# Kernel tuning notes

Measured on AMD Instinct MI355X. Metric: run time of the kernel, lower is better.

Reference implementation:

```python
import jax, jax.numpy as jnp
import numpy as np


def rotate_half(x):
    # interleaved rotate: (x0,x1,x2,x3,...) -> (-x1,x0,-x3,x2,...)
    x1 = x[..., 0::2]
    x2 = x[..., 1::2]
    return jnp.stack((-x2, x1), axis=-1).reshape(x.shape)


def setup_inputs() -> dict:
    key = jax.random.key(0)
    B, T, C, H = 8, 2048, 2048, 128
    ks = jax.random.split(key, 4)
    x = jax.random.normal(ks[0], (B, T, C), dtype=jnp.float32)
    wq = jax.random.normal(ks[1], (C, H), dtype=jnp.float32) * (C ** -0.5)
    wk = jax.random.normal(ks[2], (C, H), dtype=jnp.float32) * (C ** -0.5)
    wv = jax.random.normal(ks[3], (C, H), dtype=jnp.float32) * (C ** -0.5)
    # standard RoPE tables, interleaved pairs share a frequency
    inv_freq = 1.0 / (10000.0 ** (np.arange(0, H, 2, dtype=np.float32) / H))  # [H/2]
    ang = np.arange(T, dtype=np.float32)[:, None] * inv_freq[None, :]          # [T, H/2]
    ang = np.repeat(ang, 2, axis=-1)                                           # [T, H]
    rope_cos = jnp.asarray(np.cos(ang), dtype=jnp.float32)
    rope_sin = jnp.asarray(np.sin(ang), dtype=jnp.float32)
    return {"x": x, "wq": wq, "wk": wk, "wv": wv,
            "rope_cos": rope_cos, "rope_sin": rope_sin}


def reference(x, wq, wk, wv, rope_cos, rope_sin):
    B, T, C = x.shape
    H = wq.shape[1]
    q = x @ wq  # [B,T,H]
    k = x @ wk
    cos = rope_cos[:T][None]  # [1,T,H]
    sin = rope_sin[:T][None]
    q = q * cos + rotate_half(q) * sin
    k = k * cos + rotate_half(k) * sin
    wei = jnp.einsum('bth,bsh->bts', q, k) / (H ** 0.5)  # [B,T,T]
    causal = jnp.tril(jnp.ones((T, T), dtype=bool))
    wei = jnp.where(causal[None], wei, -jnp.inf)
    wei = jax.nn.softmax(wei, axis=-1)
    v = x @ wv  # [B,T,H]
    out = jnp.einsum('bts,bsh->bth', wei, v)
    return out
```

## Files before the change

### kernel.cpp

```cpp
#include <hip/hip_runtime.h>
#include <hip/hip_bf16.h>

typedef __attribute__((ext_vector_type(8))) short bf16x8;
typedef __attribute__((ext_vector_type(8))) unsigned short u16x8;
typedef __attribute__((ext_vector_type(4))) unsigned short u16x4;
typedef __attribute__((ext_vector_type(4))) float f32x4;

__device__ __forceinline__ unsigned short f2bf(float f) {
    __hip_bfloat16 h = __float2bfloat16(f);
    return *reinterpret_cast<unsigned short*>(&h);
}

__device__ __forceinline__ void cp16(void* lds, const void* g) {
    __builtin_amdgcn_global_load_lds(
        (const __attribute__((address_space(1))) unsigned int*)g,
        (__attribute__((address_space(3))) unsigned int*)lds, 16, 0, 0);
}

__global__ __launch_bounds__(256) void pack_w(
    const float* __restrict__ wq, const float* __restrict__ wk,
    const float* __restrict__ wv, unsigned short* __restrict__ wt)
{
    int idx = blockIdx.x * 256 + threadIdx.x;
    int n   = idx & 127;
    int k   = (idx >> 7) & 2047;
    int sel = idx >> 18;
    const float* w = (sel == 0) ? wq : (sel == 1) ? wk : wv;
    wt[(size_t)(sel * 128 + n) * 2048 + k] = f2bf(w[k * 128 + n]);
}

__global__ __launch_bounds__(256) void qkv_gemm(
    const float* __restrict__ x, const unsigned short* __restrict__ wt,
    const float* __restrict__ rc, const float* __restrict__ rs,
    unsigned short* __restrict__ Qb, unsigned short* __restrict__ Kb,
    unsigned short* __restrict__ VT)
{
    __shared__ __align__(16) unsigned short As[2][128 * 32];
    __shared__ __align__(16) unsigned short Bs[2][128 * 32];

    const int bid   = blockIdx.x;
    const int slot  = bid & 7;
    const int idx   = bid >> 3;
    const int mtile = slot + 8 * (idx / 3);
    const int ntile = idx % 3;

    const int tid  = threadIdx.x;
    const int lane = tid & 63;
    const int wid  = tid >> 6;
    const int wm   = wid >> 1, wn = wid & 1;
    const int grp  = lane >> 4, cl = lane & 15;

    const int arow0 = tid >> 2;
    const int ak8   = tid & 3;

    const float*          xbase = x  + (size_t)(mtile * 128) * 2048;
    const unsigned short* wbase = wt + (size_t)(ntile * 128) * 2048;

    float4 afl[2][2];
    u16x8  bwl[2];

    auto gload = [&](int ks) {
        int k0 = ks * 32 + ak8 * 8;
        #pragma unroll
        for (int i = 0; i < 2; ++i) {
            int row = arow0 + i * 64;
            const float* p = xbase + (size_t)row * 2048 + k0;
            afl[i][0] = *reinterpret_cast<const float4*>(p);
            afl[i][1] = *reinterpret_cast<const float4*>(p + 4);
            bwl[i]    = *reinterpret_cast<const u16x8*>(wbase + (size_t)row * 2048 + k0);
        }
    };
    auto swrite = [&](int buf) {
        #pragma unroll
        for (int i = 0; i < 2; ++i) {
            int row = arow0 + i * 64;
            u16x8 u;
            u[0] = f2bf(afl[i][0].x); u[1] = f2bf(afl[i][0].y);
            u[2] = f2bf(afl[i][0].z); u[3] = f2bf(afl[i][0].w);
            u[4] = f2bf(afl[i][1].x); u[5] = f2bf(afl[i][1].y);
            u[6] = f2bf(afl[i][1].z); u[7] = f2bf(afl[i][1].w);
            *reinterpret_cast<u16x8*>(&As[buf][row * 32 + ak8 * 8]) = u;
            *reinterpret_cast<u16x8*>(&Bs[buf][row * 32 + ak8 * 8]) = bwl[i];
        }
    };

    const f32x4 fz = {0.f, 0.f, 0.f, 0.f};
    f32x4 acc[4][4];
    #pragma unroll
    for (int mf = 0; mf < 4; ++mf)
        #pragma unroll
        for (int nf = 0; nf < 4; ++nf) acc[mf][nf] = fz;

    gload(0);
    swrite(0);
    __syncthreads();

    for (int ks = 0; ks < 64; ++ks) {
        int cur = ks & 1;
        if (ks < 63) gload(ks + 1);

        bf16x8 a[4], b[4];
        #pragma unroll
        for (int mf = 0; mf < 4; ++mf)
            a[mf] = *reinterpret_cast<const bf16x8*>(
                &As[cur][(wm * 64 + mf * 16 + cl) * 32 + grp * 8]);
        #pragma unroll
        for (int nf = 0; nf < 4; ++nf)
            b[nf] = *reinterpret_cast<const bf16x8*>(
                &Bs[cur][(wn * 64 + nf * 16 + cl) * 32 + grp * 8]);
        #pragma unroll
        for (int mf = 0; mf < 4; ++mf)
            #pragma unroll
            for (int nf = 0; nf < 4; ++nf)
                acc[mf][nf] = __builtin_amdgcn_mfma_f32_16x16x32_bf16(
                    a[mf], b[nf], acc[mf][nf], 0, 0, 0);

        if (ks < 63) swrite(cur ^ 1);
        __syncthreads();
    }

    if (ntile == 0) {
        #pragma unroll
        for (int mf = 0; mf < 4; ++mf) {
            int mrow = mtile * 128 + wm * 64 + mf * 16 + grp * 4;
            #pragma unroll
            for (int nf = 0; nf < 4; ++nf) {
                int h = wn * 64 + nf * 16 + cl;
                #pragma unroll
                for (int r = 0; r < 4; ++r) {
                    int   m   = mrow + r;
                    int   t   = m & 2047;
                    float val = acc[mf][nf][r];
                    float pr  = __shfl_xor(val, 1, 64);
                    float cs  = rc[t * 128 + h];
                    float sn  = rs[t * 128 + h];
                    float res = (h & 1) ? fmaf(val, cs, pr * sn)
                                        : fmaf(val, cs, -pr * sn);
                    Qb[(size_t)m * 128 + h] = f2bf(res);
                }
            }
        }
    } else if (ntile == 1) {
        #pragma unroll
        for (int mf = 0; mf < 4; ++mf) {
            int mrow = mtile * 128 + wm * 64 + mf * 16 + grp * 4;
            #pragma unroll
            for (int nf = 0; nf < 4; ++nf) {
                int h = wn * 64 + nf * 16 + cl;
                #pragma unroll
                for (int r = 0; r < 4; ++r) {
                    int   m   = mrow + r;
                    int   t   = m & 2047;
                    float val = acc[mf][nf][r];
                    float pr  = __shfl_xor(val, 1, 64);
                    float cs  = rc[t * 128 + h];
                    float sn  = rs[t * 128 + h];
                    float res = (h & 1) ? fmaf(val, cs, pr * sn)
                                        : fmaf(val, cs, -pr * sn);
                    int bo = h * 2;
                    int bs = (bo & 128) | ((bo & 127) ^ ((m & 7) << 4));
                    Kb[(size_t)m * 128 + (bs >> 1)] = f2bf(res);
                }
            }
        }
    } else {
        #pragma unroll
        for (int mf = 0; mf < 4; ++mf) {
            int mrow = mtile * 128 + wm * 64 + mf * 16 + grp * 4;
            int bb   = mrow >> 11;
            int t0   = mrow & 2047;
            #pragma unroll
            for (int nf = 0; nf < 4; ++nf) {
                int h = wn * 64 + nf * 16 + cl;
                u16x4 pk;
                #pragma unroll
                for (int r = 0; r < 4; ++r) pk[r] = f2bf(acc[mf][nf][r]);
                int bo = (t0 * 2) & 127;
                int bs = ((t0 * 2) & ~127) | (bo ^ ((h & 7) << 4));
                *reinterpret_cast<u16x4*>(
                    &VT[(size_t)(bb * 128 + h) * 2048 + (bs >> 1)]) = pk;
            }
        }
    }
}

__global__ __launch_bounds__(256, 2) void flash_attn(
    const unsigned short* __restrict__ Qb, const unsigned short* __restrict__ Kb,
    const unsigned short* __restrict__ VT, float* __restrict__ Op,
    float2* __restrict__ ML, float* __restrict__ out, int nchunk)
{
    __shared__ __align__(16) unsigned short Ks[2][64 * 128];
    __shared__ __align__(16) unsigned short Vs[2][128 * 64];
    __shared__ __align__(16) unsigned short Ps[4][16 * 72];

    const int g      = blockIdx.x;
    const int per_mt = 8 * nchunk;
    const int mtd    = g / per_mt;
    const int mt     = 31 - mtd;
    const int rem    = g - mtd * per_mt;
    const int c      = rem >> 3;
    const int b      = rem & 7;

    const int tid  = threadIdx.x;
    const int lane = tid & 63;
    const int w    = tid >> 6;
    const int grp  = lane >> 4, cl = lane & 15;

    const int NT   = mt + 1;
    const int T0   = (NT + 1) >> 1;
    const int tbeg = (nchunk == 2 && c == 1) ? T0 : 0;
    const int tend = (nchunk == 2 && c == 0) ? T0 : NT;

    const int   q0    = mt * 64 + w * 16;
    const float scale = 0.08838834764831845f;

    bf16x8 aq[4];
    {
        const unsigned short* qp = Qb + (size_t)(b * 2048 + q0 + cl) * 128 + grp * 8;
        #pragma unroll
        for (int kc = 0; kc < 4; ++kc)
            aq[kc] = *reinterpret_cast<const bf16x8*>(qp + kc * 32);
    }

    const f32x4 fz = {0.f, 0.f, 0.f, 0.f};
    f32x4 o[8];
    #pragma unroll
    for (int nf = 0; nf < 8; ++nf) o[nf] = fz;
    float mrun[4], lrun[4];
    #pragma unroll
    for (int r = 0; r < 4; ++r) { mrun[r] = -INFINITY; lrun[r] = 0.f; }

    const char* kgb = (const char*)(Kb + (size_t)b * 2048 * 128);
    const char* vgb = (const char*)(VT + (size_t)b * 128 * 2048);

    auto stage = [&](int d, int t) {
        const char* ks = kgb + (size_t)t * 64 * 256;
        char* kd = (char*)&Ks[d][0];
        #pragma unroll
        for (int i = 0; i < 4; ++i) {
            int off = w * 4096 + i * 1024 + lane * 16;
            cp16(kd + off, ks + off);
        }
        const char* vsb = vgb + (size_t)t * 128;
        char* vd = (char*)&Vs[d][0];
        #pragma unroll
        for (int i = 0; i < 4; ++i) {
            int off = w * 4096 + i * 1024 + lane * 16;
            cp16(vd + off, vsb + (size_t)(off >> 7) * 4096 + (off & 127));
        }
    };

    if (tbeg < tend) stage(0, tbeg);
    __syncthreads();

    int cur = 0;
    for (int t = tbeg; t < tend; ++t) {
        if (t + 1 < tend) stage(cur ^ 1, t + 1);

        const char* kb   = (const char*)&Ks[cur][0];
        const char* vb   = (const char*)&Vs[cur][0];
        const bool  diag = (t == mt);
        const int   jmax = diag ? (w + 1) : 4;

        float p[4][4];
        float mx[4];
        #pragma unroll
        for (int r = 0; r < 4; ++r) mx[r] = -INFINITY;

        #pragma unroll
        for (int j = 0; j < 4; ++j) {
            #pragma unroll
            for (int r = 0; r < 4; ++r) p[j][r] = 0.f;
            if (j < jmax) {
                int   row = j * 16 + cl;
                f32x4 s   = fz;
                #pragma unroll
                for (int kc = 0; kc < 4; ++kc) {
                    int bo = kc * 64 + grp * 16;
                    int bs = (bo & 128) | ((bo & 127) ^ ((row & 7) << 4));
                    bf16x8 kf = *reinterpret_cast<const bf16x8*>(kb + row * 256 + bs);
                    s = __builtin_amdgcn_mfma_f32_16x16x32_bf16(aq[kc], kf, s, 0, 0, 0);
                }
                #pragma unroll
                for (int r = 0; r < 4; ++r) {
                    float a = s[r] * scale;
                    if (diag && j == w && cl > grp * 4 + r) a = -INFINITY;
                    p[j][r] = a;
                    mx[r]   = fmaxf(mx[r], a);
                }
            }
        }
        #pragma unroll
        for (int d = 1; d < 16; d <<= 1)
            #pragma unroll
            for (int r = 0; r < 4; ++r)
                mx[r] = fmaxf(mx[r], __shfl_xor(mx[r], d, 64));

        float alpha[4], psum[4];
        #pragma unroll
        for (int r = 0; r < 4; ++r) {
            float mn = fmaxf(mrun[r], mx[r]);
            alpha[r] = __expf(mrun[r] - mn);
            mrun[r]  = mn;
            psum[r]  = 0.f;
        }
        #pragma unroll
        for (int j = 0; j < 4; ++j)
            if (j < jmax)
                #pragma unroll
                for (int r = 0; r < 4; ++r) {
                    p[j][r] = __expf(p[j][r] - mrun[r]);
                    psum[r] += p[j][r];
                }
        #pragma unroll
        for (int d = 1; d < 16; d <<= 1)
            #pragma unroll
            for (int r = 0; r < 4; ++r)
                psum[r] += __shfl_xor(psum[r], d, 64);
        #pragma unroll
        for (int r = 0; r < 4; ++r)
            lrun[r] = lrun[r] * alpha[r] + psum[r];
        #pragma unroll
        for (int nf = 0; nf < 8; ++nf)
            #pragma unroll
            for (int r = 0; r < 4; ++r) o[nf][r] *= alpha[r];

        char* pwb = (char*)&Ps[w][0];
        #pragma unroll
        for (int j = 0; j < 4; ++j)
            #pragma unroll
            for (int r = 0; r < 4; ++r) {
                int prow = grp * 4 + r;
                int bytec = ((j * 16 + cl) * 2) ^ ((prow & 7) << 4);
                *reinterpret_cast<unsigned short*>(pwb + prow * 144 + bytec) =
                    f2bf(p[j][r]);
            }

        const char* pb = (const char*)&Ps[w][0];
        #pragma unroll
        for (int half = 0; half < 2; ++half) {
            int pbo = half * 64 + grp * 16;
            bf16x8 pa = *reinterpret_cast<const bf16x8*>(
                pb + cl * 144 + (pbo ^ ((cl & 7) << 4)));
            #pragma unroll
            for (int nf = 0; nf < 8; ++nf) {
                int h  = nf * 16 + cl;
                int bs = (half * 64 + grp * 16) ^ ((h & 7) << 4);
                bf16x8 vf = *reinterpret_cast<const bf16x8*>(vb + h * 128 + bs);
                o[nf] = __builtin_amdgcn_mfma_f32_16x16x32_bf16(pa, vf, o[nf], 0, 0, 0);
            }
        }
        __syncthreads();
        cur ^= 1;
    }

    if (nchunk == 2) {
        #pragma unroll
        for (int nf = 0; nf < 8; ++nf)
            #pragma unroll
            for (int r = 0; r < 4; ++r) {
                size_t rowg = (size_t)c * 16384 + b * 2048 + q0 + grp * 4 + r;
                Op[rowg * 128 + nf * 16 + cl] = o[nf][r];
            }
        if (cl == 0)
            #pragma unroll
            for (int r = 0; r < 4; ++r)
                ML[(size_t)c * 16384 + b * 2048 + q0 + grp * 4 + r] =
                    make_float2(mrun[r], lrun[r]);
    } else {
        float inv[4];
        #pragma unroll
        for (int r = 0; r < 4; ++r) inv[r] = 1.0f / lrun[r];
        #pragma unroll
        for (int nf = 0; nf < 8; ++nf)
            #pragma unroll
            for (int r = 0; r < 4; ++r)
                out[(size_t)(b * 2048 + q0 + grp * 4 + r) * 128 + nf * 16 + cl] =
                    o[nf][r] * inv[r];
    }
}

__global__ __launch_bounds__(256) void merge2(
    const float* __restrict__ Op, const float2* __restrict__ ML,
    float* __restrict__ out)
{
    int idx = blockIdx.x * 256 + threadIdx.x;
    int row = idx >> 5, hq = idx & 31;
    float2 ml0 = ML[row];
    float2 ml1 = ML[16384 + row];
    float  m  = fmaxf(ml0.x, ml1.x);
    float  e0 = __expf(ml0.x - m);
    float  e1 = __expf(ml1.x - m);
    float  inv = 1.0f / (ml0.y * e0 + ml1.y * e1);
    f32x4 o0 = *reinterpret_cast<const f32x4*>(Op + (size_t)row * 128 + hq * 4);
    f32x4 o1 = *reinterpret_cast<const f32x4*>(Op + ((size_t)16384 + row) * 128 + hq * 4);
    f32x4 res;
    #pragma unroll
    for (int i = 0; i < 4; ++i) res[i] = (o0[i] * e0 + o1[i] * e1) * inv;
    *reinterpret_cast<f32x4*>(out + (size_t)row * 128 + hq * 4) = res;
}

extern "C" void kernel_launch(void* const* d_in, const int* in_sizes, int n_in,
                              void* d_out, int out_size, void* d_ws, size_t ws_size,
                              hipStream_t stream)
{
    const float* x  = (const float*)d_in[0];
    const float* wq = (const float*)d_in[1];
    const float* wk = (const float*)d_in[2];
    const float* wv = (const float*)d_in[3];
    const float* rc = (const float*)d_in[4];
    const float* rs = (const float*)d_in[5];
    float* out = (float*)d_out;

    char* ws = (char*)d_ws;
    unsigned short* wt = (unsigned short*)(ws);
    unsigned short* Qb = (unsigned short*)(ws + (2u  << 20));
    unsigned short* Kb = (unsigned short*)(ws + (6u  << 20));
    unsigned short* VT = (unsigned short*)(ws + (10u << 20));
    float*          Op = (float*)        (ws + (14u << 20));
    float2*         ML = (float2*)       (ws + (30u << 20));

    const int nchunk = (ws_size >= ((size_t)31 << 20)) ? 2 : 1;

    pack_w    <<<3072, 256, 0, stream>>>(wq, wk, wv, wt);
    qkv_gemm  <<<384,  256, 0, stream>>>(x, wt, rc, rs, Qb, Kb, VT);
    flash_attn<<<32 * 8 * nchunk, 256, 0, stream>>>(Qb, Kb, VT, Op, ML, out, nchunk);
    if (nchunk == 2)
        merge2<<<2048, 256, 0, stream>>>(Op, ML, out);
}
```

Before: 105.0 us.

## Split QKV GEMM along K into two halves with fp16 partials and merge kernels

The QKV projection GEMM is split along the reduction dimension into two halves, doubling the block count from 384 to 768 for better occupancy across the CUs. Each half writes fp16 partial sums to workspace. Separate merge kernels then add the partials, apply RoPE and swizzle Q/K, and transpose V. The B operand is now staged with direct global-to-LDS loads. In exchange this adds extra kernel launches, a round trip of partials through memory, and some fp16 rounding on the partials; the path is used only when the workspace is at least 39 MB.

```diff
diff --git a/kernel.cpp b/kernel.cpp
--- a/kernel.cpp
+++ b/kernel.cpp
@@ -1,5 +1,6 @@
 #include <hip/hip_runtime.h>
 #include <hip/hip_bf16.h>
+#include <hip/hip_fp16.h>
 
 typedef __attribute__((ext_vector_type(8))) short bf16x8;
 typedef __attribute__((ext_vector_type(8))) unsigned short u16x8;
@@ -9,6 +10,14 @@
 __device__ __forceinline__ unsigned short f2bf(float f) {
     __hip_bfloat16 h = __float2bfloat16(f);
     return *reinterpret_cast<unsigned short*>(&h);
+}
+__device__ __forceinline__ unsigned short f2h(float f) {
+    __half h = __float2half(f);
+    return *reinterpret_cast<unsigned short*>(&h);
+}
+__device__ __forceinline__ float h2f(unsigned short u) {
+    __half h = *reinterpret_cast<__half*>(&u);
+    return __half2float(h);
 }
 
 __device__ __forceinline__ void cp16(void* lds, const void* g) {
@@ -29,7 +38,191 @@
     wt[(size_t)(sel * 128 + n) * 2048 + k] = f2bf(w[k * 128 + n]);
 }
 
-__global__ __launch_bounds__(256) void qkv_gemm(
+__global__ __launch_bounds__(256) void qkv_gemm_ks(
+    const float* __restrict__ x, const unsigned short* __restrict__ wt,
+    unsigned short* __restrict__ Pp)
+{
+    __shared__ __align__(16) unsigned short As[2][128 * 32];
+    __shared__ __align__(16) unsigned short Bs[2][128 * 32];
+
+    const int bid   = blockIdx.x;
+    const int slot  = bid & 7;
+    const int idx   = bid >> 3;
+    const int mtile = slot + 8 * (idx / 6);
+    const int sub   = idx % 6;
+    const int ntile = sub >> 1;
+    const int kc    = sub & 1;
+
+    const int tid  = threadIdx.x;
+    const int lane = tid & 63;
+    const int w    = tid >> 6;
+    const int wm   = w >> 1, wn = w & 1;
+    const int grp  = lane >> 4, cl = lane & 15;
+
+    const int arow0 = tid >> 2;
+    const int ak8   = tid & 3;
+
+    const float* xbase = x + (size_t)(mtile * 128) * 2048 + kc * 1024;
+    const char*  wbyte = (const char*)(wt + (size_t)(ntile * 128) * 2048 + kc * 1024);
+
+    float4 afl[2][2];
+
+    auto gloadA = [&](int ks) {
+        int k0 = ks * 32 + ak8 * 8;
+        #pragma unroll
+        for (int i = 0; i < 2; ++i) {
+            const float* p = xbase + (size_t)(arow0 + i * 64) * 2048 + k0;
+            afl[i][0] = *reinterpret_cast<const float4*>(p);
+            afl[i][1] = *reinterpret_cast<const float4*>(p + 4);
+        }
+    };
+    auto swriteA = [&](int buf) {
+        #pragma unroll
+        for (int i = 0; i < 2; ++i) {
+            int row = arow0 + i * 64;
+            u16x8 u;
+            u[0] = f2bf(afl[i][0].x); u[1] = f2bf(afl[i][0].y);
+            u[2] = f2bf(afl[i][0].z); u[3] = f2bf(afl[i][0].w);
+            u[4] = f2bf(afl[i][1].x); u[5] = f2bf(afl[i][1].y);
+            u[6] = f2bf(afl[i][1].z); u[7] = f2bf(afl[i][1].w);
+            *reinterpret_cast<u16x8*>(&As[buf][row * 32 + ak8 * 8]) = u;
+        }
+    };
+    auto stageB = [&](int buf, int ks) {
+        #pragma unroll
+        for (int i = 0; i < 2; ++i) {
+            int   r0  = w * 32 + i * 16;
+            char* dst = (char*)&Bs[buf][0] + r0 * 64;
+            const char* src = wbyte + (size_t)(r0 + (lane >> 2)) * 4096
+                              + ks * 64 + (lane & 3) * 16;
+            cp16(dst, src);
+        }
+    };
+
+    const f32x4 fz = {0.f, 0.f, 0.f, 0.f};
+    f32x4 acc[4][4];
+    #pragma unroll
+    for (int mf = 0; mf < 4; ++mf)
+        #pragma unroll
+        for (int nf = 0; nf < 4; ++nf) acc[mf][nf] = fz;
+
+    gloadA(0);
+    stageB(0, 0);
+    swriteA(0);
+    __syncthreads();
+
+    for (int ks = 0; ks < 32; ++ks) {
+        int cur = ks & 1;
+        if (ks < 31) { gloadA(ks + 1); stageB(cur ^ 1, ks + 1); }
+
+        bf16x8 a[4], b[4];
+        #pragma unroll
+        for (int mf = 0; mf < 4; ++mf)
+            a[mf] = *reinterpret_cast<const bf16x8*>(
+                &As[cur][(wm * 64 + mf * 16 + cl) * 32 + grp * 8]);
+        #pragma unroll
+        for (int nf = 0; nf < 4; ++nf)
+            b[nf] = *reinterpret_cast<const bf16x8*>(
+                &Bs[cur][(wn * 64 + nf * 16 + cl) * 32 + grp * 8]);
+        #pragma unroll
+        for (int mf = 0; mf < 4; ++mf)
+            #pragma unroll
+            for (int nf = 0; nf < 4; ++nf)
+                acc[mf][nf] = __builtin_amdgcn_mfma_f32_16x16x32_bf16(
+                    a[mf], b[nf], acc[mf][nf], 0, 0, 0);
+
+        if (ks < 31) swriteA(cur ^ 1);
+        __syncthreads();
+    }
+
+    unsigned short* pp = Pp + (size_t)kc * 16384 * 384;
+    #pragma unroll
+    for (int mf = 0; mf < 4; ++mf) {
+        int mrow = mtile * 128 + wm * 64 + mf * 16 + grp * 4;
+        #pragma unroll
+        for (int nf = 0; nf < 4; ++nf) {
+            int ncol = ntile * 128 + wn * 64 + nf * 16 + cl;
+            #pragma unroll
+            for (int r = 0; r < 4; ++r)
+                pp[(size_t)(mrow + r) * 384 + ncol] = f2h(acc[mf][nf][r]);
+        }
+    }
+}
+
+__global__ __launch_bounds__(256) void merge_qk(
+    const unsigned short* __restrict__ Pp, const float* __restrict__ rc,
+    const float* __restrict__ rs, unsigned short* __restrict__ Qb,
+    unsigned short* __restrict__ Kb)
+{
+    int idx  = blockIdx.x * 256 + threadIdx.x;
+    int m    = idx >> 5;
+    int col0 = (idx & 31) * 8;
+    const unsigned short* p0 = Pp + (size_t)m * 384 + col0;
+    u16x8 a = *reinterpret_cast<const u16x8*>(p0);
+    u16x8 b = *reinterpret_cast<const u16x8*>(p0 + (size_t)16384 * 384);
+    float s[8];
+    #pragma unroll
+    for (int j = 0; j < 8; ++j) s[j] = h2f(a[j]) + h2f(b[j]);
+
+    int t  = m & 2047;
+    int h0 = col0 & 127;
+    u16x8 ob;
+    #pragma unroll
+    for (int i = 0; i < 4; ++i) {
+        float c  = rc[t * 128 + h0 + 2 * i];
+        float sn = rs[t * 128 + h0 + 2 * i];
+        ob[2 * i]     = f2bf(s[2 * i] * c - s[2 * i + 1] * sn);
+        ob[2 * i + 1] = f2bf(s[2 * i + 1] * c + s[2 * i] * sn);
+    }
+    if (col0 < 128) {
+        *reinterpret_cast<u16x8*>(Qb + (size_t)m * 128 + col0) = ob;
+    } else {
+        int bo = (col0 - 128) * 2;
+        int bs = (bo & 128) | ((bo & 127) ^ ((m & 7) << 4));
+        *reinterpret_cast<u16x8*>((char*)Kb + (size_t)m * 256 + bs) = ob;
+    }
+}
+
+__global__ __launch_bounds__(256) void merge_v(
+    const unsigned short* __restrict__ Pp, unsigned short* __restrict__ VT)
+{
+    __shared__ unsigned short L[128 * 80];
+
+    const int tid = threadIdx.x;
+    const int m0  = blockIdx.x * 64;
+
+    {
+        int i  = tid >> 2;
+        int c0 = (tid & 3) * 32;
+        const unsigned short* p0 = Pp + (size_t)(m0 + i) * 384 + 256 + c0;
+        #pragma unroll
+        for (int cc = 0; cc < 4; ++cc) {
+            u16x8 a = *reinterpret_cast<const u16x8*>(p0 + cc * 8);
+            u16x8 b = *reinterpret_cast<const u16x8*>(p0 + cc * 8 + (size_t)16384 * 384);
+            #pragma unroll
+            for (int j = 0; j < 8; ++j)
+                L[(c0 + cc * 8 + j) * 80 + i] = f2bf(h2f(a[j]) + h2f(b[j]));
+        }
+    }
+    __syncthreads();
+    {
+        int vh  = tid >> 1;
+        int th0 = (tid & 1) * 32;
+        int bb  = m0 >> 11;
+        int tb  = m0 & 2047;
+        char* vrow = (char*)VT + (size_t)(bb * 128 + vh) * 4096;
+        #pragma unroll
+        for (int cc = 0; cc < 4; ++cc) {
+            int tl = th0 + cc * 8;
+            u16x8 v = *reinterpret_cast<const u16x8*>(&L[vh * 80 + tl]);
+            int bo = (tb + tl) * 2;
+            int bs = (bo & ~127) | ((bo & 127) ^ ((vh & 7) << 4));
+            *reinterpret_cast<u16x8*>(vrow + bs) = v;
+        }
+    }
+}
+
+__global__ __launch_bounds__(256) void qkv_gemm_mono(
     const float* __restrict__ x, const unsigned short* __restrict__ wt,
     const float* __restrict__ rc, const float* __restrict__ rs,
     unsigned short* __restrict__ Qb, unsigned short* __restrict__ Kb,
@@ -49,7 +242,6 @@
     const int wid  = tid >> 6;
     const int wm   = wid >> 1, wn = wid & 1;
     const int grp  = lane >> 4, cl = lane & 15;
-
     const int arow0 = tid >> 2;
     const int ak8   = tid & 3;
 
@@ -91,14 +283,11 @@
         #pragma unroll
         for (int nf = 0; nf < 4; ++nf) acc[mf][nf] = fz;
 
-    gload(0);
-    swrite(0);
-    __syncthreads();
+    gload(0); swrite(0); __syncthreads();
 
     for (int ks = 0; ks < 64; ++ks) {
         int cur = ks & 1;
         if (ks < 63) gload(ks + 1);
-
         bf16x8 a[4], b[4];
         #pragma unroll
         for (int mf = 0; mf < 4; ++mf)
@@ -114,7 +303,6 @@
             for (int nf = 0; nf < 4; ++nf)
                 acc[mf][nf] = __builtin_amdgcn_mfma_f32_16x16x32_bf16(
                     a[mf], b[nf], acc[mf][nf], 0, 0, 0);
-
         if (ks < 63) swrite(cur ^ 1);
         __syncthreads();
     }
@@ -413,18 +601,31 @@
     float* out = (float*)d_out;
 
     char* ws = (char*)d_ws;
+    const size_t MB = 1u << 20;
     unsigned short* wt = (unsigned short*)(ws);
-    unsigned short* Qb = (unsigned short*)(ws + (2u  << 20));
-    unsigned short* Kb = (unsigned short*)(ws + (6u  << 20));
-    unsigned short* VT = (unsigned short*)(ws + (10u << 20));
-    float*          Op = (float*)        (ws + (14u << 20));
-    float2*         ML = (float2*)       (ws + (30u << 20));
-
-    const int nchunk = (ws_size >= ((size_t)31 << 20)) ? 2 : 1;
-
-    pack_w    <<<3072, 256, 0, stream>>>(wq, wk, wv, wt);
-    qkv_gemm  <<<384,  256, 0, stream>>>(x, wt, rc, rs, Qb, Kb, VT);
-    flash_attn<<<32 * 8 * nchunk, 256, 0, stream>>>(Qb, Kb, VT, Op, ML, out, nchunk);
-    if (nchunk == 2)
-        merge2<<<2048, 256, 0, stream>>>(Op, ML, out);
-}
+    unsigned short* Qb = (unsigned short*)(ws + 2 * MB);
+    unsigned short* Kb = (unsigned short*)(ws + 6 * MB);
+    unsigned short* VT = (unsigned short*)(ws + 10 * MB);
+
+    pack_w<<<3072, 256, 0, stream>>>(wq, wk, wv, wt);
+
+    if (ws_size >= 39 * MB) {
+        unsigned short* Pp = (unsigned short*)(ws + 14 * MB);
+        float*          Op = (float*)        (ws + 14 * MB);
+        float2*         ML = (float2*)       (ws + 30 * MB);
+
+        qkv_gemm_ks<<<768,  256, 0, stream>>>(x, wt, Pp);
+        merge_qk   <<<2048, 256, 0, stream>>>(Pp, rc, rs, Qb, Kb);
+        merge_v    <<<256,  256, 0, stream>>>(Pp, VT);
+        flash_attn <<<512,  256, 0, stream>>>(Qb, Kb, VT, Op, ML, out, 2);
+        merge2     <<<2048, 256, 0, stream>>>(Op, ML, out);
+    } else {
+        float*  Op = (float*) (ws + 14 * MB);
+        float2* ML = (float2*)(ws + 30 * MB);
+        const int nchunk = (ws_size >= (size_t)31 * MB) ? 2 : 1;
+        qkv_gemm_mono<<<384, 256, 0, stream>>>(x, wt, rc, rs, Qb, Kb, VT);
+        flash_attn<<<32 * 8 * nchunk, 256, 0, stream>>>(Qb, Kb, VT, Op, ML, out, nchunk);
+        if (nchunk == 2)
+            merge2<<<2048, 256, 0, stream>>>(Op, ML, out);
+    }
+}
```

After: 118.9 us. 13.2% more time.

## Compute full QKV row tile per block with async LDS weight staging

Applied to the files above, without the earlier changes.

The QKV GEMM now assigns each block a 64-row tile of x and all 384 output columns (Q, K and V together), so x is read and converted to bf16 once instead of three times. Weight tiles are streamed straight into a triple-buffered LDS ring with global_load_lds and an XOR swizzle, and the x tile is double-buffered in registers with manual vmcnt waits. The grid drops from 384 to 256 blocks and accumulators grow to 4x6 per wave, raising register and LDS pressure. The epilogue picks the Q, K or V path per fragment.

```diff
diff --git a/kernel.cpp b/kernel.cpp
--- a/kernel.cpp
+++ b/kernel.cpp
@@ -35,150 +35,145 @@
     unsigned short* __restrict__ Qb, unsigned short* __restrict__ Kb,
     unsigned short* __restrict__ VT)
 {
-    __shared__ __align__(16) unsigned short As[2][128 * 32];
-    __shared__ __align__(16) unsigned short Bs[2][128 * 32];
-
-    const int bid   = blockIdx.x;
-    const int slot  = bid & 7;
-    const int idx   = bid >> 3;
-    const int mtile = slot + 8 * (idx / 3);
-    const int ntile = idx % 3;
-
+    __shared__ __align__(16) unsigned short As[2][64 * 32];
+    __shared__ __align__(16) unsigned short Bs[3][384 * 32];
+
+    const int mtile = blockIdx.x;
     const int tid  = threadIdx.x;
     const int lane = tid & 63;
-    const int wid  = tid >> 6;
-    const int wm   = wid >> 1, wn = wid & 1;
+    const int w    = tid >> 6;
     const int grp  = lane >> 4, cl = lane & 15;
 
-    const int arow0 = tid >> 2;
-    const int ak8   = tid & 3;
-
-    const float*          xbase = x  + (size_t)(mtile * 128) * 2048;
-    const unsigned short* wbase = wt + (size_t)(ntile * 128) * 2048;
-
-    float4 afl[2][2];
-    u16x8  bwl[2];
-
-    auto gload = [&](int ks) {
-        int k0 = ks * 32 + ak8 * 8;
-        #pragma unroll
-        for (int i = 0; i < 2; ++i) {
-            int row = arow0 + i * 64;
-            const float* p = xbase + (size_t)row * 2048 + k0;
-            afl[i][0] = *reinterpret_cast<const float4*>(p);
-            afl[i][1] = *reinterpret_cast<const float4*>(p + 4);
-            bwl[i]    = *reinterpret_cast<const u16x8*>(wbase + (size_t)row * 2048 + k0);
-        }
+    const int arow = tid >> 2;
+    const int ac   = tid & 3;
+    const float* asrc = x + ((size_t)(mtile * 64) + arow) * 2048 + ac * 8;
+    const int    awsl = ac ^ ((arow >> 1) & 3);
+    unsigned short* awd[2] = { &As[0][arow * 32 + awsl * 8],
+                               &As[1][arow * 32 + awsl * 8] };
+
+    float4 bufA0[2], bufA1[2];
+
+    auto loadA = [&](float4* buf, int ks) {
+        const float* p = asrc + ks * 32;
+        buf[0] = *reinterpret_cast<const float4*>(p);
+        buf[1] = *reinterpret_cast<const float4*>(p + 4);
     };
-    auto swrite = [&](int buf) {
-        #pragma unroll
-        for (int i = 0; i < 2; ++i) {
-            int row = arow0 + i * 64;
-            u16x8 u;
-            u[0] = f2bf(afl[i][0].x); u[1] = f2bf(afl[i][0].y);
-            u[2] = f2bf(afl[i][0].z); u[3] = f2bf(afl[i][0].w);
-            u[4] = f2bf(afl[i][1].x); u[5] = f2bf(afl[i][1].y);
-            u[6] = f2bf(afl[i][1].z); u[7] = f2bf(afl[i][1].w);
-            *reinterpret_cast<u16x8*>(&As[buf][row * 32 + ak8 * 8]) = u;
-            *reinterpret_cast<u16x8*>(&Bs[buf][row * 32 + ak8 * 8]) = bwl[i];
-        }
+    auto writeA = [&](const float4* buf, int which) {
+        u16x8 u;
+        u[0]=f2bf(buf[0].x); u[1]=f2bf(buf[0].y); u[2]=f2bf(buf[0].z); u[3]=f2bf(buf[0].w);
+        u[4]=f2bf(buf[1].x); u[5]=f2bf(buf[1].y); u[6]=f2bf(buf[1].z); u[7]=f2bf(buf[1].w);
+        *reinterpret_cast<u16x8*>(which ? awd[1] : awd[0]) = u;
     };
+    auto stageB = [&](int dbuf, int ks) {
+        #pragma unroll
+        for (int i = 0; i < 6; ++i) {
+            int idx  = tid + i * 256;
+            int n    = idx >> 2;
+            int csl  = idx & 3;
+            int csrc = csl ^ ((n >> 1) & 3);
+            cp16((char*)&Bs[dbuf][0] + idx * 16,
+                 (const char*)wt + (size_t)n * 4096 + ks * 64 + csrc * 16);
+        }
+    };
 
     const f32x4 fz = {0.f, 0.f, 0.f, 0.f};
-    f32x4 acc[4][4];
+    f32x4 acc[4][6];
     #pragma unroll
     for (int mf = 0; mf < 4; ++mf)
         #pragma unroll
-        for (int nf = 0; nf < 4; ++nf) acc[mf][nf] = fz;
-
-    gload(0);
-    swrite(0);
-    __syncthreads();
-
-    for (int ks = 0; ks < 64; ++ks) {
-        int cur = ks & 1;
-        if (ks < 63) gload(ks + 1);
-
-        bf16x8 a[4], b[4];
+        for (int nf = 0; nf < 6; ++nf) acc[mf][nf] = fz;
+
+    loadA(bufA0, 0);
+    loadA(bufA1, 1);
+    stageB(0, 0);
+    stageB(1, 1);
+    writeA(bufA0, 0);
+    asm volatile("s_waitcnt vmcnt(6)" ::: "memory");
+    asm volatile("s_waitcnt lgkmcnt(0)" ::: "memory");
+    __builtin_amdgcn_s_barrier();
+
+    auto step = [&](int t, float4* lb, const float4* wb) {
+        if (t < 62) { loadA(lb, t + 2); stageB((t + 2) % 3, t + 2); }
+
+        bf16x8 a[4], b[6];
+        {
+            const unsigned short* ab = &As[t & 1][0];
+            const unsigned short* bb = &Bs[t % 3][0];
+            #pragma unroll
+            for (int mf = 0; mf < 4; ++mf) {
+                int row = mf * 16 + cl;
+                int sl  = grp ^ ((row >> 1) & 3);
+                a[mf] = *reinterpret_cast<const bf16x8*>(ab + row * 32 + sl * 8);
+            }
+            #pragma unroll
+            for (int nf = 0; nf < 6; ++nf) {
+                int n  = w * 96 + nf * 16 + cl;
+                int sl = grp ^ ((n >> 1) & 3);
+                b[nf] = *reinterpret_cast<const bf16x8*>(bb + n * 32 + sl * 8);
+            }
+        }
+        if (t < 63) writeA(wb, (t + 1) & 1);
+
         #pragma unroll
         for (int mf = 0; mf < 4; ++mf)
-            a[mf] = *reinterpret_cast<const bf16x8*>(
-                &As[cur][(wm * 64 + mf * 16 + cl) * 32 + grp * 8]);
-        #pragma unroll
-        for (int nf = 0; nf < 4; ++nf)
-            b[nf] = *reinterpret_cast<const bf16x8*>(
-                &Bs[cur][(wn * 64 + nf * 16 + cl) * 32 + grp * 8]);
-        #pragma unroll
-        for (int mf = 0; mf < 4; ++mf)
-            #pragma unroll
-            for (int nf = 0; nf < 4; ++nf)
+            #pragma unroll
+            for (int nf = 0; nf < 6; ++nf)
                 acc[mf][nf] = __builtin_amdgcn_mfma_f32_16x16x32_bf16(
                     a[mf], b[nf], acc[mf][nf], 0, 0, 0);
 
-        if (ks < 63) swrite(cur ^ 1);
-        __syncthreads();
+        if (t < 62) {
+            asm volatile("s_waitcnt vmcnt(8)" ::: "memory");
+        } else if (t < 63) {
+            asm volatile("s_waitcnt vmcnt(0)" ::: "memory");
+        }
+        if (t < 63) {
+            asm volatile("s_waitcnt lgkmcnt(0)" ::: "memory");
+            __builtin_amdgcn_s_barrier();
+        }
+    };
+
+    for (int tt = 0; tt < 32; ++tt) {
+        step(2 * tt,     bufA0, bufA1);
+        step(2 * tt + 1, bufA1, bufA0);
     }
 
-    if (ntile == 0) {
-        #pragma unroll
-        for (int mf = 0; mf < 4; ++mf) {
-            int mrow = mtile * 128 + wm * 64 + mf * 16 + grp * 4;
-            #pragma unroll
-            for (int nf = 0; nf < 4; ++nf) {
-                int h = wn * 64 + nf * 16 + cl;
+    #pragma unroll
+    for (int mf = 0; mf < 4; ++mf) {
+        int mrow = mtile * 64 + mf * 16 + grp * 4;
+        int bb   = mrow >> 11;
+        #pragma unroll
+        for (int nf = 0; nf < 6; ++nf) {
+            int nbase = w * 96 + nf * 16;
+            int sel   = nbase >> 7;
+            int h     = (nbase & 127) + cl;
+            if (sel < 2) {
                 #pragma unroll
                 for (int r = 0; r < 4; ++r) {
                     int   m   = mrow + r;
-                    int   t   = m & 2047;
+                    int   tr  = m & 2047;
                     float val = acc[mf][nf][r];
                     float pr  = __shfl_xor(val, 1, 64);
-                    float cs  = rc[t * 128 + h];
-                    float sn  = rs[t * 128 + h];
+                    float cs  = rc[tr * 128 + h];
+                    float sn  = rs[tr * 128 + h];
                     float res = (h & 1) ? fmaf(val, cs, pr * sn)
                                         : fmaf(val, cs, -pr * sn);
-                    Qb[(size_t)m * 128 + h] = f2bf(res);
+                    if (sel == 0) {
+                        Qb[(size_t)m * 128 + h] = f2bf(res);
+                    } else {
+                        int bo = h * 2;
+                        int bs = (bo & 128) | ((bo & 127) ^ ((m & 7) << 4));
+                        *(unsigned short*)((char*)Kb + (size_t)m * 256 + bs) = f2bf(res);
+                    }
                 }
-            }
-        }
-    } else if (ntile == 1) {
-        #pragma unroll
-        for (int mf = 0; mf < 4; ++mf) {
-            int mrow = mtile * 128 + wm * 64 + mf * 16 + grp * 4;
-            #pragma unroll
-            for (int nf = 0; nf < 4; ++nf) {
-                int h = wn * 64 + nf * 16 + cl;
-                #pragma unroll
-                for (int r = 0; r < 4; ++r) {
-                    int   m   = mrow + r;
-                    int   t   = m & 2047;
-                    float val = acc[mf][nf][r];
-                    float pr  = __shfl_xor(val, 1, 64);
-                    float cs  = rc[t * 128 + h];
-                    float sn  = rs[t * 128 + h];
-                    float res = (h & 1) ? fmaf(val, cs, pr * sn)
-                                        : fmaf(val, cs, -pr * sn);
-                    int bo = h * 2;
-                    int bs = (bo & 128) | ((bo & 127) ^ ((m & 7) << 4));
-                    Kb[(size_t)m * 128 + (bs >> 1)] = f2bf(res);
-                }
-            }
-        }
-    } else {
-        #pragma unroll
-        for (int mf = 0; mf < 4; ++mf) {
-            int mrow = mtile * 128 + wm * 64 + mf * 16 + grp * 4;
-            int bb   = mrow >> 11;
-            int t0   = mrow & 2047;
-            #pragma unroll
-            for (int nf = 0; nf < 4; ++nf) {
-                int h = wn * 64 + nf * 16 + cl;
+            } else {
                 u16x4 pk;
                 #pragma unroll
                 for (int r = 0; r < 4; ++r) pk[r] = f2bf(acc[mf][nf][r]);
+                int t0 = mrow & 2047;
                 int bo = (t0 * 2) & 127;
                 int bs = ((t0 * 2) & ~127) | (bo ^ ((h & 7) << 4));
                 *reinterpret_cast<u16x4*>(
-                    &VT[(size_t)(bb * 128 + h) * 2048 + (bs >> 1)]) = pk;
+                    (char*)VT + (size_t)(bb * 128 + h) * 4096 + bs) = pk;
             }
         }
     }
@@ -413,17 +408,18 @@
     float* out = (float*)d_out;
 
     char* ws = (char*)d_ws;
+    const size_t MB = 1u << 20;
     unsigned short* wt = (unsigned short*)(ws);
-    unsigned short* Qb = (unsigned short*)(ws + (2u  << 20));
-    unsigned short* Kb = (unsigned short*)(ws + (6u  << 20));
-    unsigned short* VT = (unsigned short*)(ws + (10u << 20));
-    float*          Op = (float*)        (ws + (14u << 20));
-    float2*         ML = (float2*)       (ws + (30u << 20));
-
-    const int nchunk = (ws_size >= ((size_t)31 << 20)) ? 2 : 1;
-
-    pack_w    <<<3072, 256, 0, stream>>>(wq, wk, wv, wt);
-    qkv_gemm  <<<384,  256, 0, stream>>>(x, wt, rc, rs, Qb, Kb, VT);
+    unsigned short* Qb = (unsigned short*)(ws + 2 * MB);
+    unsigned short* Kb = (unsigned short*)(ws + 6 * MB);
+    unsigned short* VT = (unsigned short*)(ws + 10 * MB);
+    float*          Op = (float*)        (ws + 14 * MB);
+    float2*         ML = (float2*)       (ws + 30 * MB);
+
+    const int nchunk = (ws_size >= (size_t)31 * MB) ? 2 : 1;
+
+    pack_w  <<<3072, 256, 0, stream>>>(wq, wk, wv, wt);
+    qkv_gemm<<<256,  256, 0, stream>>>(x, wt, rc, rs, Qb, Kb, VT);
     flash_attn<<<32 * 8 * nchunk, 256, 0, stream>>>(Qb, Kb, VT, Op, ML, out, nchunk);
     if (nchunk == 2)
         merge2<<<2048, 256, 0, stream>>>(Op, ML, out);
```

Measured after the change: 151.5 us. 44.3% more time.

## Stage QKV GEMM operands via direct global-to-LDS loads with swizzled layout

Applied to the files above, without the earlier changes.

The QKV projection GEMM now copies x (kept as fp32) and the packed bf16 weights straight from global memory into LDS using global_load_lds 16-byte transfers, replacing the register-staged load, convert and store path. The bf16 conversion of x moves to the point where fragments are read from LDS. An XOR swizzle is applied to both tiles to reduce bank conflicts. This removes register pressure and VALU work in the prefetch path, but doubles the LDS footprint for the A tile and repeats the fp32-to-bf16 conversion on every fragment read, since each A element is read by both wn warps.

```diff
diff --git a/kernel.cpp b/kernel.cpp
--- a/kernel.cpp
+++ b/kernel.cpp
@@ -35,7 +35,7 @@
     unsigned short* __restrict__ Qb, unsigned short* __restrict__ Kb,
     unsigned short* __restrict__ VT)
 {
-    __shared__ __align__(16) unsigned short As[2][128 * 32];
+    __shared__ __align__(16) float          As[2][128 * 32];
     __shared__ __align__(16) unsigned short Bs[2][128 * 32];
 
     const int bid   = blockIdx.x;
@@ -50,37 +50,25 @@
     const int wm   = wid >> 1, wn = wid & 1;
     const int grp  = lane >> 4, cl = lane & 15;
 
-    const int arow0 = tid >> 2;
-    const int ak8   = tid & 3;
-
-    const float*          xbase = x  + (size_t)(mtile * 128) * 2048;
-    const unsigned short* wbase = wt + (size_t)(ntile * 128) * 2048;
-
-    float4 afl[2][2];
-    u16x8  bwl[2];
-
-    auto gload = [&](int ks) {
-        int k0 = ks * 32 + ak8 * 8;
-        #pragma unroll
-        for (int i = 0; i < 2; ++i) {
-            int row = arow0 + i * 64;
-            const float* p = xbase + (size_t)row * 2048 + k0;
-            afl[i][0] = *reinterpret_cast<const float4*>(p);
-            afl[i][1] = *reinterpret_cast<const float4*>(p + 4);
-            bwl[i]    = *reinterpret_cast<const u16x8*>(wbase + (size_t)row * 2048 + k0);
-        }
-    };
-    auto swrite = [&](int buf) {
-        #pragma unroll
-        for (int i = 0; i < 2; ++i) {
-            int row = arow0 + i * 64;
-            u16x8 u;
-            u[0] = f2bf(afl[i][0].x); u[1] = f2bf(afl[i][0].y);
-            u[2] = f2bf(afl[i][0].z); u[3] = f2bf(afl[i][0].w);
-            u[4] = f2bf(afl[i][1].x); u[5] = f2bf(afl[i][1].y);
-            u[6] = f2bf(afl[i][1].z); u[7] = f2bf(afl[i][1].w);
-            *reinterpret_cast<u16x8*>(&As[buf][row * 32 + ak8 * 8]) = u;
-            *reinterpret_cast<u16x8*>(&Bs[buf][row * 32 + ak8 * 8]) = bwl[i];
+    const float*          xb = x  + (size_t)(mtile * 128) * 2048;
+    const unsigned short* wb = wt + (size_t)(ntile * 128) * 2048;
+
+    auto stage = [&](int buf, int ks) {
+        #pragma unroll
+        for (int it = 0; it < 4; ++it) {
+            int i   = tid + it * 256;
+            int row = i >> 3;
+            int cs  = (i & 7) ^ (row & 6);
+            cp16((char*)&As[buf][0] + i * 16,
+                 xb + (size_t)row * 2048 + ks * 32 + cs * 4);
+        }
+        #pragma unroll
+        for (int it = 0; it < 2; ++it) {
+            int i  = tid + it * 256;
+            int n  = i >> 2;
+            int cs = (i & 3) ^ ((n >> 1) & 3);
+            cp16((char*)&Bs[buf][0] + i * 16,
+                 (const char*)(wb + (size_t)n * 2048 + ks * 32) + cs * 16);
         }
     };
 
@@ -91,23 +79,34 @@
         #pragma unroll
         for (int nf = 0; nf < 4; ++nf) acc[mf][nf] = fz;
 
-    gload(0);
-    swrite(0);
+    stage(0, 0);
     __syncthreads();
 
     for (int ks = 0; ks < 64; ++ks) {
         int cur = ks & 1;
-        if (ks < 63) gload(ks + 1);
+        if (ks < 63) stage(cur ^ 1, ks + 1);
 
         bf16x8 a[4], b[4];
         #pragma unroll
-        for (int mf = 0; mf < 4; ++mf)
-            a[mf] = *reinterpret_cast<const bf16x8*>(
-                &As[cur][(wm * 64 + mf * 16 + cl) * 32 + grp * 8]);
-        #pragma unroll
-        for (int nf = 0; nf < 4; ++nf)
-            b[nf] = *reinterpret_cast<const bf16x8*>(
-                &Bs[cur][(wn * 64 + nf * 16 + cl) * 32 + grp * 8]);
+        for (int mf = 0; mf < 4; ++mf) {
+            int row = wm * 64 + mf * 16 + cl;
+            int pr  = grp ^ ((row >> 1) & 3);
+            const float* ap = &As[cur][row * 32 + pr * 8];
+            f32x4 lo = *reinterpret_cast<const f32x4*>(ap);
+            f32x4 hi = *reinterpret_cast<const f32x4*>(ap + 4);
+            bf16x8 av;
+            av[0] = (short)f2bf(lo[0]); av[1] = (short)f2bf(lo[1]);
+            av[2] = (short)f2bf(lo[2]); av[3] = (short)f2bf(lo[3]);
+            av[4] = (short)f2bf(hi[0]); av[5] = (short)f2bf(hi[1]);
+            av[6] = (short)f2bf(hi[2]); av[7] = (short)f2bf(hi[3]);
+            a[mf] = av;
+        }
+        #pragma unroll
+        for (int nf = 0; nf < 4; ++nf) {
+            int n  = wn * 64 + nf * 16 + cl;
+            int sl = grp ^ ((n >> 1) & 3);
+            b[nf] = *reinterpret_cast<const bf16x8*>(&Bs[cur][n * 32 + sl * 8]);
+        }
         #pragma unroll
         for (int mf = 0; mf < 4; ++mf)
             #pragma unroll
@@ -115,7 +114,6 @@
                 acc[mf][nf] = __builtin_amdgcn_mfma_f32_16x16x32_bf16(
                     a[mf], b[nf], acc[mf][nf], 0, 0, 0);
 
-        if (ks < 63) swrite(cur ^ 1);
         __syncthreads();
     }
 
@@ -159,7 +157,7 @@
                                         : fmaf(val, cs, -pr * sn);
                     int bo = h * 2;
                     int bs = (bo & 128) | ((bo & 127) ^ ((m & 7) << 4));
-                    Kb[(size_t)m * 128 + (bs >> 1)] = f2bf(res);
+                    *(unsigned short*)((char*)Kb + (size_t)m * 256 + bs) = f2bf(res);
                 }
             }
         }
@@ -178,7 +176,7 @@
                 int bo = (t0 * 2) & 127;
                 int bs = ((t0 * 2) & ~127) | (bo ^ ((h & 7) << 4));
                 *reinterpret_cast<u16x4*>(
-                    &VT[(size_t)(bb * 128 + h) * 2048 + (bs >> 1)]) = pk;
+                    (char*)VT + (size_t)(bb * 128 + h) * 4096 + bs) = pk;
             }
         }
     }
@@ -413,17 +411,18 @@
     float* out = (float*)d_out;
 
     char* ws = (char*)d_ws;
+    const size_t MB = 1u << 20;
     unsigned short* wt = (unsigned short*)(ws);
-    unsigned short* Qb = (unsigned short*)(ws + (2u  << 20));
-    unsigned short* Kb = (unsigned short*)(ws + (6u  << 20));
-    unsigned short* VT = (unsigned short*)(ws + (10u << 20));
-    float*          Op = (float*)        (ws + (14u << 20));
-    float2*         ML = (float2*)       (ws + (30u << 20));
-
-    const int nchunk = (ws_size >= ((size_t)31 << 20)) ? 2 : 1;
-
-    pack_w    <<<3072, 256, 0, stream>>>(wq, wk, wv, wt);
-    qkv_gemm  <<<384,  256, 0, stream>>>(x, wt, rc, rs, Qb, Kb, VT);
+    unsigned short* Qb = (unsigned short*)(ws + 2 * MB);
+    unsigned short* Kb = (unsigned short*)(ws + 6 * MB);
+    unsigned short* VT = (unsigned short*)(ws + 10 * MB);
+    float*          Op = (float*)        (ws + 14 * MB);
+    float2*         ML = (float2*)       (ws + 30 * MB);
+
+    const int nchunk = (ws_size >= (size_t)31 * MB) ? 2 : 1;
+
+    pack_w  <<<3072, 256, 0, stream>>>(wq, wk, wv, wt);
+    qkv_gemm<<<384,  256, 0, stream>>>(x, wt, rc, rs, Qb, Kb, VT);
     flash_attn<<<32 * 8 * nchunk, 256, 0, stream>>>(Qb, Kb, VT, Op, ML, out, nchunk);
     if (nchunk == 2)
         merge2<<<2048, 256, 0, stream>>>(Op, ML, out);
```

Result: slower. 128.7 us (+22.6%).
